# Kernel optimization log

Measured on AMD Instinct MI355X. Metric: run time of the kernel, lower is better.

The kernel has to match this reference:

```python
import jax, jax.numpy as jnp
import numpy as np

RRELU_SLOPE = (1.0 / 8.0 + 1.0 / 3.0) / 2.0  # F.rrelu eval-mode slope = 11/48

N_NODES = 50000
N_EDGES = 800000
H_DIM = 128
N_REL2 = 460  # 2 * num_rels
T_DIM = 64
BATCH = 1024
SEQ_LEN = 10


def _rrelu(x):
    return jnp.where(x >= 0, x, x * RRELU_SLOPE)


def _rgcn_layer(h, rel, src, dst, etype, norm, has_in, w_neigh, loop_w, evolve_w):
    # UnionRGCNLayer (comp='sub'): msg = (h_src - rel[etype]) @ W_neigh, sum into dst, * 1/indeg
    msg = (h[src] - rel[etype]) @ w_neigh                                # [E, h]
    agg = jax.ops.segment_sum(msg, dst, num_segments=h.shape[0]) * norm  # [N, h]
    # self-loop: nodes with in-degree>0 use loop_weight, isolated nodes use evolve_loop_weight
    loop_msg = jnp.where(has_in[:, None], h @ loop_w, h @ evolve_w)
    return _rrelu(agg + loop_msg)  # dropout p=0.0 -> identity


def setup_inputs() -> dict:
    key = jax.random.key(0)
    ks = jax.random.split(key, 12)
    sc = 1.0 / np.sqrt(H_DIM)
    return {
        "h": jax.random.normal(ks[0], (N_NODES, H_DIM), jnp.float32),
        "rel_embeds": jax.random.normal(ks[1], (N_REL2, H_DIM), jnp.float32),
        "w_neigh1": jax.random.normal(ks[2], (H_DIM, H_DIM), jnp.float32) * sc,
        "loop_w1": jax.random.normal(ks[3], (H_DIM, H_DIM), jnp.float32) * sc,
        "evolve_w1": jax.random.normal(ks[4], (H_DIM, H_DIM), jnp.float32) * sc,
        "w_neigh2": jax.random.normal(ks[5], (H_DIM, H_DIM), jnp.float32) * sc,
        "loop_w2": jax.random.normal(ks[6], (H_DIM, H_DIM), jnp.float32) * sc,
        "evolve_w2": jax.random.normal(ks[7], (H_DIM, H_DIM), jnp.float32) * sc,
        "t_w": jax.random.normal(ks[8], (T_DIM,), jnp.float32),
        "t_b": jax.random.normal(ks[9], (T_DIM,), jnp.float32),
        "src": jax.random.randint(ks[10], (N_EDGES,), 0, N_NODES, jnp.int32),
        "dst": jax.random.randint(ks[11], (N_EDGES,), 0, N_NODES, jnp.int32),
        "etype": jax.random.randint(jax.random.fold_in(key, 1), (N_EDGES,), 0, N_REL2, jnp.int32),
        "node_ids_graph": jax.random.randint(jax.random.fold_in(key, 2), (BATCH, SEQ_LEN), 0, N_NODES + 1, jnp.int32),
        "times": jax.random.randint(jax.random.fold_in(key, 3), (BATCH, SEQ_LEN), 0, 1000, jnp.int32),
    }


def reference(h, rel_embeds, w_neigh1, loop_w1, evolve_w1, w_neigh2, loop_w2, evolve_w2,
              t_w, t_b, src, dst, etype, node_ids_graph, times):
    N, H = h.shape
    deg = jax.ops.segment_sum(jnp.ones_like(dst, dtype=h.dtype), dst, num_segments=N)
    has_in = deg > 0
    norm = (1.0 / jnp.maximum(deg, 1.0))[:, None]  # dgl 'norm' = 1/in-degree

    h1 = _rgcn_layer(h, rel_embeds, src, dst, etype, norm, has_in, w_neigh1, loop_w1, evolve_w1)
    h2 = _rgcn_layer(h1, rel_embeds, src, dst, etype, norm, has_in, w_neigh2, loop_w2, evolve_w2)

    # concat zero padding row, then irregular gather by node_ids_graph
    embeds = jnp.concatenate([h2, jnp.zeros((1, H), h.dtype)], axis=0)  # [N+1, h]
    s_embed = embeds[node_ids_graph]                                    # [B, L, h]

    B, L = node_ids_graph.shape
    t = times.reshape(-1, 1).astype(h.dtype)                            # [B*L, 1]
    time_emb = jnp.cos(t * t_w + t_b).reshape(B, L, t_w.shape[0])       # [B, L, t_dim]

    return jnp.concatenate([s_embed, time_emb], axis=-1)  # dropout p=0.0 -> identity
```

## Files before the change

kernel.cpp:

```cpp
#include <hip/hip_runtime.h>


#define HD 128
#define TD 64
#define BSH 7
#define NBLK 256
constexpr float SLOPE = 11.0f / 48.0f;

typedef unsigned short u16;
typedef unsigned int u32;
typedef short bf16x8 __attribute__((ext_vector_type(8)));
typedef float f32x4 __attribute__((ext_vector_type(4)));

__device__ __forceinline__ float bf2f(u16 b) {
    return __uint_as_float(((u32)b) << 16);
}
__device__ __forceinline__ u16 f2bf(float f) {
    u32 u = __float_as_uint(f);
    u += 0x7FFFu + ((u >> 16) & 1u);
    return (u16)(u >> 16);
}

__global__ __launch_bounds__(256)
void conv_kernel(const float4* __restrict__ in, ushort4* __restrict__ out, int n4)
{
    int i = blockIdx.x * 256 + threadIdx.x;
    if (i >= n4) return;
    float4 v = in[i];
    ushort4 o;
    o.x = f2bf(v.x); o.y = f2bf(v.y); o.z = f2bf(v.z); o.w = f2bf(v.w);
    out[i] = o;
}

__global__ __launch_bounds__(256)
void bt_kernel(const float* __restrict__ Wn, const float* __restrict__ Lw,
               u16* __restrict__ BT)
{
    int idx = blockIdx.x * 256 + threadIdx.x;
    int c = idx >> 8, k = idx & 255;
    float v = (k < HD) ? Wn[k * HD + c] : Lw[(k - HD) * HD + c];
    BT[(size_t)c * 256 + k] = f2bf(v);
}

__global__ __launch_bounds__(256)
void cntA(const int* __restrict__ dst, int E, int* __restrict__ cnt, int NBKT)
{
    __shared__ int hist[512];
    const int b = blockIdx.x, t = threadIdx.x;
    for (int i = t; i < NBKT; i += 256) hist[i] = 0;
    __syncthreads();
    const int chunk = (E + NBLK - 1) / NBLK;
    const int e0 = b * chunk;
    const int e1 = (e0 + chunk < E) ? e0 + chunk : E;
    for (int e = e0 + t; e < e1; e += 256)
        atomicAdd(&hist[dst[e] >> BSH], 1);
    __syncthreads();
    for (int i = t; i < NBKT; i += 256)
        cnt[(size_t)i * NBLK + b] = hist[i];
}

__global__ __launch_bounds__(256)
void scan1_kernel(const int* __restrict__ v, int* __restrict__ bsum, int M)
{
    __shared__ int red[256];
    const int b = blockIdx.x, t = threadIdx.x;
    int s = 0;
    #pragma unroll
    for (int j = 0; j < 4; j++) {
        int i = b * 1024 + j * 256 + t;
        if (i < M) s += v[i];
    }
    red[t] = s;
    __syncthreads();
    for (int off = 128; off; off >>= 1) {
        if (t < off) red[t] += red[t + off];
        __syncthreads();
    }
    if (t == 0) bsum[b] = red[0];
}

__global__ __launch_bounds__(64)
void scan2_kernel(int* __restrict__ bsum, int NB, int* __restrict__ totalOut)
{
    if (threadIdx.x == 0 && blockIdx.x == 0) {
        int acc = 0;
        for (int b = 0; b < NB; b++) { int x = bsum[b]; bsum[b] = acc; acc += x; }
        *totalOut = acc;
    }
}

__global__ __launch_bounds__(1024)
void scan3_kernel(const int* __restrict__ v, const int* __restrict__ bsum,
                  int* __restrict__ start, int M)
{
    __shared__ int buf[1024];
    const int b = blockIdx.x, t = threadIdx.x;
    const int i = b * 1024 + t;
    const int x = (i < M) ? v[i] : 0;
    buf[t] = x;
    __syncthreads();
    for (int off = 1; off < 1024; off <<= 1) {
        int y = (t >= off) ? buf[t - off] : 0;
        __syncthreads();
        buf[t] += y;
        __syncthreads();
    }
    if (i < M) start[i] = bsum[b] + buf[t] - x;
}

__global__ __launch_bounds__(256)
void passA2(const int* __restrict__ src, const int* __restrict__ dst,
            const int* __restrict__ ety, const int* __restrict__ start,
            u32* __restrict__ elistA, int E, int NBKT)
{
    __shared__ int cur[512];
    const int b = blockIdx.x, t = threadIdx.x;
    for (int i = t; i < NBKT; i += 256) cur[i] = start[(size_t)i * NBLK + b];
    __syncthreads();
    const int chunk = (E + NBLK - 1) / NBLK;
    const int e0 = b * chunk;
    const int e1 = (e0 + chunk < E) ? e0 + chunk : E;
    for (int e = e0 + t; e < e1; e += 256) {
        int d = dst[e];
        u32 entry = ((u32)(d & 127) << 25) | ((u32)ety[e] << 16) | (u32)src[e];
        int pos = atomicAdd(&cur[d >> BSH], 1);
        elistA[pos] = entry;
    }
}

__global__ __launch_bounds__(256)
void passB(const u32* __restrict__ elistA, const int* __restrict__ start,
           u32* __restrict__ elist, int* __restrict__ rowstart, int Nn, int E,
           int NBKT)
{
    __shared__ int cnt[128];
    __shared__ int ofs[128];
    const int b = blockIdx.x, t = threadIdx.x;
    const int beg = start[(size_t)b * NBLK];
    const int end = (b + 1 < NBKT) ? start[(size_t)(b + 1) * NBLK] : E;
    if (t < 128) cnt[t] = 0;
    __syncthreads();
    for (int i = beg + t; i < end; i += 256)
        atomicAdd(&cnt[elistA[i] >> 25], 1);
    __syncthreads();
    if (t == 0) {
        int acc = 0;
        for (int j = 0; j < 128; j++) { ofs[j] = acc; acc += cnt[j]; }
    }
    __syncthreads();
    const int n0 = b << BSH;
    if (t < 128 && n0 + t < Nn) rowstart[n0 + t] = beg + ofs[t];
    if (b == 0 && t == 0) rowstart[Nn] = E;
    __syncthreads();
    for (int i = beg + t; i < end; i += 256) {
        u32 v = elistA[i];
        int p = atomicAdd(&ofs[v >> 25], 1);
        elist[beg + p] = v & 0x01ffffffu;
    }
}

__global__ __launch_bounds__(64)
void gagg_kernel(const u32* __restrict__ hbf2, const u32* __restrict__ relbf2,
                 const u32* __restrict__ elist, const int* __restrict__ rowstart,
                 u32* __restrict__ Sn2, int Nn)
{
    int n = blockIdx.x;
    if (n >= Nn) return;
    int c = threadIdx.x;
    int beg = rowstart[n], end = rowstart[n + 1];
    float ae[8] = {}, ao[8] = {};
    int i = beg;
    for (; i + 8 <= end; i += 8) {
        #pragma unroll
        for (int j = 0; j < 8; j++) {
            u32 v = elist[i + j];
            u32 hv = hbf2[(size_t)(v & 0xffffu) * 64 + c];
            u32 rv = relbf2[(size_t)(v >> 16) * 64 + c];
            ae[j] += bf2f((u16)(hv & 0xffffu)) - bf2f((u16)(rv & 0xffffu));
            ao[j] += bf2f((u16)(hv >> 16)) - bf2f((u16)(rv >> 16));
        }
    }
    for (; i < end; i++) {
        u32 v = elist[i];
        u32 hv = hbf2[(size_t)(v & 0xffffu) * 64 + c];
        u32 rv = relbf2[(size_t)(v >> 16) * 64 + c];
        ae[0] += bf2f((u16)(hv & 0xffffu)) - bf2f((u16)(rv & 0xffffu));
        ao[0] += bf2f((u16)(hv >> 16)) - bf2f((u16)(rv >> 16));
    }
    float se = ((ae[0] + ae[1]) + (ae[2] + ae[3])) + ((ae[4] + ae[5]) + (ae[6] + ae[7]));
    float so = ((ao[0] + ao[1]) + (ao[2] + ao[3])) + ((ao[4] + ao[5]) + (ao[6] + ao[7]));
    int d = end - beg;
    float nrm = 1.0f / (float)((d > 0) ? d : 1);
    se *= nrm; so *= nrm;
    Sn2[(size_t)n * 64 + c] = (u32)f2bf(se) | ((u32)f2bf(so) << 16);
}

__global__ __launch_bounds__(256)
void mfma_kernel(const u16* __restrict__ Sn, const u16* __restrict__ Hn,
                 const u16* __restrict__ BT, const int* __restrict__ rowstart,
                 const float* __restrict__ Ew, u16* __restrict__ Out, int Nn)
{
    __shared__ u16 BTs[128 * 256];

    const int tid = threadIdx.x;
    #pragma unroll
    for (int j = 0; j < 16; j++) {
        int chunk = tid + j * 256;
        int byte = chunk << 4;
        int row = byte >> 9;
        int sw = byte ^ ((row & 7) << 4);
        *(ulonglong2*)((char*)BTs + sw) = *(const ulonglong2*)((const char*)BT + byte);
    }
    __syncthreads();

    const int lane = tid & 63;
    const int wave = tid >> 6;
    const int row0 = blockIdx.x * 128 + wave * 32;
    const int lr = lane & 15;
    const int lk = (lane >> 4) * 8;

    f32x4 acc[2][8];
    #pragma unroll
    for (int m = 0; m < 2; m++)
        #pragma unroll
        for (int n = 0; n < 8; n++)
            acc[m][n] = (f32x4){0.f, 0.f, 0.f, 0.f};

    int r0 = row0 + lr;      if (r0 >= Nn) r0 = Nn - 1;
    int r1 = row0 + 16 + lr; if (r1 >= Nn) r1 = Nn - 1;
    const size_t rb0 = (size_t)r0 * HD, rb1 = (size_t)r1 * HD;

    #pragma unroll
    for (int ks = 0; ks < 8; ks++) {
        const u16* A = (ks < 4) ? Sn : Hn;
        const int kc = (ks & 3) * 32 + lk;
        bf16x8 a0 = *(const bf16x8*)&A[rb0 + kc];
        bf16x8 a1 = *(const bf16x8*)&A[rb1 + kc];
        #pragma unroll
        for (int nf = 0; nf < 8; nf++) {
            const int brow = nf * 16 + lr;
            int boff = (brow << 9) + ((ks * 32 + lk) << 1);
            boff ^= (brow & 7) << 4;
            bf16x8 b = *(const bf16x8*)((const char*)BTs + boff);
            acc[0][nf] = __builtin_amdgcn_mfma_f32_16x16x32_bf16(a0, b, acc[0][nf], 0, 0, 0);
            acc[1][nf] = __builtin_amdgcn_mfma_f32_16x16x32_bf16(a1, b, acc[1][nf], 0, 0, 0);
        }
    }

    #pragma unroll
    for (int mf = 0; mf < 2; mf++) {
        #pragma unroll
        for (int r = 0; r < 4; r++) {
            const int row = row0 + mf * 16 + (lane >> 4) * 4 + r;
            if (row >= Nn) continue;
            const int d = rowstart[row + 1] - rowstart[row];
            #pragma unroll
            for (int nf = 0; nf < 8; nf++) {
                const int col = nf * 16 + lr;
                float o = acc[mf][nf][r];
                if (d == 0) {
                    o = 0.f;
                    for (int k = 0; k < HD; k++)
                        o = fmaf(bf2f(Hn[(size_t)row * HD + k]), Ew[(size_t)k * HD + col], o);
                }
                o = (o >= 0.f) ? o : o * SLOPE;
                Out[(size_t)row * HD + col] = f2bf(o);
            }
        }
    }
}

__global__ __launch_bounds__(192)
void out_kernel(const u16* __restrict__ h2, const int* __restrict__ ids,
                const int* __restrict__ tms,
                const float* __restrict__ tw, const float* __restrict__ tb,
                float* __restrict__ out, int R, int Nn)
{
    int r = blockIdx.x;
    int c = threadIdx.x;
    if (r >= R) return;
    float v;
    if (c < HD) {
        int id = ids[r];
        v = (id >= 0 && id < Nn) ? bf2f(h2[(size_t)id * HD + c]) : 0.0f;
    } else {
        int j = c - HD;
        v = cosf((float)tms[r] * tw[j] + tb[j]);
    }
    out[(size_t)r * (HD + TD) + c] = v;
}

extern "C" void kernel_launch(void* const* d_in, const int* in_sizes, int n_in,
                              void* d_out, int out_size, void* d_ws, size_t ws_size,
                              hipStream_t stream)
{
    const float* h   = (const float*)d_in[0];
    const float* rel = (const float*)d_in[1];
    const float* wn1 = (const float*)d_in[2];
    const float* lw1 = (const float*)d_in[3];
    const float* ew1 = (const float*)d_in[4];
    const float* wn2 = (const float*)d_in[5];
    const float* lw2 = (const float*)d_in[6];
    const float* ew2 = (const float*)d_in[7];
    const float* tw  = (const float*)d_in[8];
    const float* tb  = (const float*)d_in[9];
    const int* src = (const int*)d_in[10];
    const int* dst = (const int*)d_in[11];
    const int* ety = (const int*)d_in[12];
    const int* ids = (const int*)d_in[13];
    const int* tms = (const int*)d_in[14];

    const int Nn  = in_sizes[0] / HD;
    const int E   = in_sizes[10];
    const int R   = in_sizes[13];
    const int NR2 = in_sizes[1] / HD;
    const int NBKT = (Nn + 127) >> BSH;
    const int M = NBKT * NBLK;
    const int NBS = (M + 1023) / 1024;

    char* ws = (char*)d_ws;
    const size_t cntB  = ((size_t)M * 4 + 255) & ~(size_t)255;
    const size_t bsB   = ((size_t)NBS * 4 + 255) & ~(size_t)255;
    const size_t stB   = (((size_t)M + 1) * 4 + 255) & ~(size_t)255;
    const size_t rsB   = (((size_t)Nn + 1) * 4 + 255) & ~(size_t)255;
    int* cnt      = (int*)(ws);
    int* bsum     = (int*)(ws + cntB);
    int* start    = (int*)(ws + cntB + bsB);
    int* rowstart = (int*)(ws + cntB + bsB + stB);
    char* p       = ws + cntB + bsB + stB + rsB;
    u32* elistA = (u32*)p;   p += ((size_t)E * 4 + 255) & ~(size_t)255;
    u32* elist  = (u32*)p;   p += ((size_t)E * 4 + 255) & ~(size_t)255;
    u16* hbf    = (u16*)p;   p += (size_t)Nn * HD * 2;
    u16* h1bf   = (u16*)p;   p += (size_t)Nn * HD * 2;
    u16* Sn     = (u16*)p;   p += (size_t)Nn * HD * 2;
    u16* h2bf   = (u16*)p;   p += (size_t)Nn * HD * 2;
    u16* relbf  = (u16*)p;   p += ((size_t)NR2 * HD * 2 + 255) & ~(size_t)255;
    u16* BT1    = (u16*)p;   p += HD * 256 * 2;
    u16* BT2    = (u16*)p;

    const int n4 = Nn * HD / 4;
    const int r4 = NR2 * HD / 4;
    const int gb = (Nn + 127) / 128;

    conv_kernel<<<(n4 + 255) / 256, 256, 0, stream>>>((const float4*)h, (ushort4*)hbf, n4);
    conv_kernel<<<(r4 + 255) / 256, 256, 0, stream>>>((const float4*)rel, (ushort4*)relbf, r4);
    bt_kernel<<<128, 256, 0, stream>>>(wn1, lw1, BT1);
    bt_kernel<<<128, 256, 0, stream>>>(wn2, lw2, BT2);

    cntA<<<NBLK, 256, 0, stream>>>(dst, E, cnt, NBKT);
    scan1_kernel<<<NBS, 256, 0, stream>>>(cnt, bsum, M);
    scan2_kernel<<<1, 64, 0, stream>>>(bsum, NBS, &start[M]);
    scan3_kernel<<<NBS, 1024, 0, stream>>>(cnt, bsum, start, M);
    passA2<<<NBLK, 256, 0, stream>>>(src, dst, ety, start, elistA, E, NBKT);
    passB<<<NBKT, 256, 0, stream>>>(elistA, start, elist, rowstart, Nn, E, NBKT);

    gagg_kernel<<<Nn, 64, 0, stream>>>((const u32*)hbf, (const u32*)relbf,
                                       elist, rowstart, (u32*)Sn, Nn);
    mfma_kernel<<<gb, 256, 0, stream>>>(Sn, hbf, BT1, rowstart, ew1, h1bf, Nn);

    gagg_kernel<<<Nn, 64, 0, stream>>>((const u32*)h1bf, (const u32*)relbf,
                                       elist, rowstart, (u32*)Sn, Nn);
    mfma_kernel<<<gb, 256, 0, stream>>>(Sn, h1bf, BT2, rowstart, ew2, h2bf, Nn);

    out_kernel<<<R, 192, 0, stream>>>(h2bf, ids, tms, tw, tb, (float*)d_out, R, Nn);
}
```

Measured before the change: 148.6 us.

## Pack gather-aggregate nodes per block, merge weight transposes, flatten output kernel

Each gagg block now handles four nodes with 256 threads instead of one node per 64-thread block. This cuts the number of blocks and the scheduling overhead in the two edge-aggregation passes. The two bt_kernel launches are merged into one, out_kernel uses a flat 256-thread grid over all output elements, and the edge-sorting block count NBLK is halved. The flat output indexing adds a 64-bit divide per element, and fewer sorting blocks may reduce parallelism in cntA and passA2.

Result: slower. 181.3 us (+22.0%).

```diff
diff --git a/kernel.cpp b/kernel.cpp
--- a/kernel.cpp
+++ b/kernel.cpp
@@ -4,7 +4,7 @@
 #define HD 128
 #define TD 64
 #define BSH 7
-#define NBLK 256
+#define NBLK 128
 constexpr float SLOPE = 11.0f / 48.0f;
 
 typedef unsigned short u16;
@@ -33,11 +33,17 @@
 }
 
 __global__ __launch_bounds__(256)
-void bt_kernel(const float* __restrict__ Wn, const float* __restrict__ Lw,
-               u16* __restrict__ BT)
+void bt_kernel(const float* __restrict__ wn1, const float* __restrict__ lw1,
+               const float* __restrict__ wn2, const float* __restrict__ lw2,
+               u16* __restrict__ BT1, u16* __restrict__ BT2)
 {
     int idx = blockIdx.x * 256 + threadIdx.x;
-    int c = idx >> 8, k = idx & 255;
+    int which = idx >> 15;
+    int j = idx & 32767;
+    int c = j >> 8, k = j & 255;
+    const float* Wn = which ? wn2 : wn1;
+    const float* Lw = which ? lw2 : lw1;
+    u16* BT = which ? BT2 : BT1;
     float v = (k < HD) ? Wn[k * HD + c] : Lw[(k - HD) * HD + c];
     BT[(size_t)c * 256 + k] = f2bf(v);
 }
@@ -159,14 +165,14 @@
     }
 }
 
-__global__ __launch_bounds__(64)
+__global__ __launch_bounds__(256)
 void gagg_kernel(const u32* __restrict__ hbf2, const u32* __restrict__ relbf2,
                  const u32* __restrict__ elist, const int* __restrict__ rowstart,
                  u32* __restrict__ Sn2, int Nn)
 {
-    int n = blockIdx.x;
+    int n = blockIdx.x * 4 + (threadIdx.x >> 6);
     if (n >= Nn) return;
-    int c = threadIdx.x;
+    int c = threadIdx.x & 63;
     int beg = rowstart[n], end = rowstart[n + 1];
     float ae[8] = {}, ao[8] = {};
     int i = beg;
@@ -270,15 +276,16 @@
     }
 }
 
-__global__ __launch_bounds__(192)
+__global__ __launch_bounds__(256)
 void out_kernel(const u16* __restrict__ h2, const int* __restrict__ ids,
                 const int* __restrict__ tms,
                 const float* __restrict__ tw, const float* __restrict__ tb,
-                float* __restrict__ out, int R, int Nn)
-{
-    int r = blockIdx.x;
-    int c = threadIdx.x;
-    if (r >= R) return;
+                float* __restrict__ out, long total, int Nn)
+{
+    long i = (long)blockIdx.x * 256 + threadIdx.x;
+    if (i >= total) return;
+    long r = i / (HD + TD);
+    int  c = (int)(i - r * (HD + TD));
     float v;
     if (c < HD) {
         int id = ids[r];
@@ -287,7 +294,7 @@
         int j = c - HD;
         v = cosf((float)tms[r] * tw[j] + tb[j]);
     }
-    out[(size_t)r * (HD + TD) + c] = v;
+    out[i] = v;
 }
 
 extern "C" void kernel_launch(void* const* d_in, const int* in_sizes, int n_in,
@@ -341,11 +348,11 @@
     const int n4 = Nn * HD / 4;
     const int r4 = NR2 * HD / 4;
     const int gb = (Nn + 127) / 128;
+    const long outN = (long)R * (HD + TD);
 
     conv_kernel<<<(n4 + 255) / 256, 256, 0, stream>>>((const float4*)h, (ushort4*)hbf, n4);
     conv_kernel<<<(r4 + 255) / 256, 256, 0, stream>>>((const float4*)rel, (ushort4*)relbf, r4);
-    bt_kernel<<<128, 256, 0, stream>>>(wn1, lw1, BT1);
-    bt_kernel<<<128, 256, 0, stream>>>(wn2, lw2, BT2);
+    bt_kernel<<<256, 256, 0, stream>>>(wn1, lw1, wn2, lw2, BT1, BT2);
 
     cntA<<<NBLK, 256, 0, stream>>>(dst, E, cnt, NBKT);
     scan1_kernel<<<NBS, 256, 0, stream>>>(cnt, bsum, M);
@@ -354,13 +361,14 @@
     passA2<<<NBLK, 256, 0, stream>>>(src, dst, ety, start, elistA, E, NBKT);
     passB<<<NBKT, 256, 0, stream>>>(elistA, start, elist, rowstart, Nn, E, NBKT);
 
-    gagg_kernel<<<Nn, 64, 0, stream>>>((const u32*)hbf, (const u32*)relbf,
-                                       elist, rowstart, (u32*)Sn, Nn);
+    gagg_kernel<<<(Nn + 3) / 4, 256, 0, stream>>>((const u32*)hbf, (const u32*)relbf,
+                                                  elist, rowstart, (u32*)Sn, Nn);
     mfma_kernel<<<gb, 256, 0, stream>>>(Sn, hbf, BT1, rowstart, ew1, h1bf, Nn);
 
-    gagg_kernel<<<Nn, 64, 0, stream>>>((const u32*)h1bf, (const u32*)relbf,
-                                       elist, rowstart, (u32*)Sn, Nn);
+    gagg_kernel<<<(Nn + 3) / 4, 256, 0, stream>>>((const u32*)h1bf, (const u32*)relbf,
+                                                  elist, rowstart, (u32*)Sn, Nn);
     mfma_kernel<<<gb, 256, 0, stream>>>(Sn, h1bf, BT2, rowstart, ew2, h2bf, Nn);
 
-    out_kernel<<<R, 192, 0, stream>>>(h2bf, ids, tms, tw, tb, (float*)d_out, R, Nn);
-}
+    out_kernel<<<(int)((outN + 255) / 256), 256, 0, stream>>>(h2bf, ids, tms, tw, tb,
+                                                              (float*)d_out, outN, Nn);
+}
```
